# Kernel optimization log

Hardware: AMD Instinct MI355X
Metric: run time of the kernel (lower is better)

The kernel has to match this reference:

```python
import jax, jax.numpy as jnp
import numpy as np

WS = 7          # window size
SHIFT = 3       # shift size (SW-MSA)
NH = 4          # num heads
EPS = 1e-5      # LayerNorm eps (torch default)


def _rel_pos_index(ws):
    coords = np.stack(np.meshgrid(np.arange(ws), np.arange(ws), indexing='ij'))  # (2, ws, ws)
    cf = coords.reshape(2, -1)                      # (2, ws*ws)
    rel = cf[:, :, None] - cf[:, None, :]           # (2, N, N)
    rel = rel.transpose(1, 2, 0)
    rel[:, :, 0] += ws - 1
    rel[:, :, 1] += ws - 1
    rel[:, :, 0] *= 2 * ws - 1
    return jnp.asarray(rel.sum(-1))                 # (N, N) int

REL_IDX = _rel_pos_index(WS)


def _shift_mask(Hp, Wp, ws, shift):
    """Standard Swin attention mask for shifted windows: (nW, N, N) float32."""
    img = np.zeros((1, Hp, Wp, 1), dtype=np.float32)
    cnt = 0
    sl = (slice(0, -ws), slice(-ws, -shift), slice(-shift, None))
    for h in sl:
        for w in sl:
            img[:, h, w, :] = cnt
            cnt += 1
    win = img.reshape(1, Hp // ws, ws, Wp // ws, ws, 1).transpose(0, 1, 3, 2, 4, 5)
    win = win.reshape(-1, ws * ws)                  # (nW, N)
    m = win[:, None, :] - win[:, :, None]
    return jnp.asarray(np.where(m != 0, -100.0, 0.0).astype(np.float32))


def _ln(x, g, b):
    mu = jnp.mean(x, -1, keepdims=True)
    var = jnp.mean(jnp.square(x - mu), -1, keepdims=True)
    return (x - mu) * jax.lax.rsqrt(var + EPS) * g + b


def _win_partition(x, ws):
    B, H, W, C = x.shape
    x = x.reshape(B, H // ws, ws, W // ws, ws, C).transpose(0, 1, 3, 2, 4, 5)
    return x.reshape(-1, ws * ws, C)


def _win_reverse(w, ws, B, H, W):
    C = w.shape[-1]
    x = w.reshape(B, H // ws, W // ws, ws, ws, C).transpose(0, 1, 3, 2, 4, 5)
    return x.reshape(B, H, W, C)


def setup_inputs() -> dict:
    key = jax.random.key(0)
    ks = jax.random.split(key, 12)
    B, H, W, C = 16, 112, 112, 128
    hid = 4 * C
    std = 0.02
    inp = {
        'x': jax.random.normal(ks[0], (B, H * W, C), jnp.float32),
        'H': H, 'W': W,
        'attn_mask': _shift_mask(H, W, WS, SHIFT),
        'ln1_g': jnp.ones((C,), jnp.float32),
        'ln1_b': jnp.zeros((C,), jnp.float32),
        'qkv_w': jax.random.normal(ks[1], (3 * C, C), jnp.float32) * std,
        'qkv_b': jnp.zeros((3 * C,), jnp.float32),
        'rel_bias_table': jax.random.normal(ks[2], ((2 * WS - 1) ** 2, NH), jnp.float32) * std,
        'proj_w': jax.random.normal(ks[3], (C, C), jnp.float32) * std,
        'proj_b': jnp.zeros((C,), jnp.float32),
        'ln2_g': jnp.ones((C,), jnp.float32),
        'ln2_b': jnp.zeros((C,), jnp.float32),
        'fc1_w': jax.random.normal(ks[4], (hid, C), jnp.float32) * std,
        'fc1_b': jnp.zeros((hid,), jnp.float32),
        'fc2_w': jax.random.normal(ks[5], (C, hid), jnp.float32) * std,
        'fc2_b': jnp.zeros((C,), jnp.float32),
    }
    return inp


def reference(x, H, W, attn_mask, ln1_g, ln1_b, qkv_w, qkv_b, rel_bias_table,
              proj_w, proj_b, ln2_g, ln2_b, fc1_w, fc1_b, fc2_w, fc2_b):
    B, L, C = x.shape
    N = WS * WS
    hd = C // NH
    scale = hd ** -0.5

    shortcut = x
    h = _ln(x, ln1_g, ln1_b).reshape(B, H, W, C)
    # H, W chosen divisible by WS -> no padding branch needed
    h = jnp.roll(h, shift=(-SHIFT, -SHIFT), axis=(1, 2))
    xw = _win_partition(h, WS)                      # (B_, N, C), B_ = B*nW
    B_ = xw.shape[0]
    nW = attn_mask.shape[0]

    qkv = xw @ qkv_w.T + qkv_b                      # (B_, N, 3C)
    qkv = qkv.reshape(B_, N, 3, NH, hd).transpose(2, 0, 3, 1, 4)
    q, k, v = qkv[0], qkv[1], qkv[2]                # (B_, NH, N, hd)

    attn = jnp.einsum('bhnd,bhmd->bhnm', q, k) * scale
    bias = rel_bias_table[REL_IDX]                  # (N, N, NH)
    attn = attn + bias.transpose(2, 0, 1)[None]     # (B_, NH, N, N)
    attn = attn.reshape(B_ // nW, nW, NH, N, N) + attn_mask[None, :, None]
    attn = jax.nn.softmax(attn.reshape(B_, NH, N, N), axis=-1)

    o = jnp.einsum('bhnm,bhmd->bhnd', attn, v)      # (B_, NH, N, hd)
    o = o.transpose(0, 2, 1, 3).reshape(B_, N, C)
    o = o @ proj_w.T + proj_b

    h = _win_reverse(o, WS, B, H, W)
    h = jnp.roll(h, shift=(SHIFT, SHIFT), axis=(1, 2))
    x1 = shortcut + h.reshape(B, L, C)

    f = _ln(x1, ln2_g, ln2_b)
    f = jax.nn.gelu(f @ fc1_w.T + fc1_b, approximate=False)
    f = f @ fc2_w.T + fc2_b
    return x1 + f
```

## Files before the change

kernel.cpp:

```cpp
#include <hip/hip_runtime.h>
#include <hip/hip_bf16.h>
#include <math.h>

#define B_IMG 16
#define HH 112
#define WW_ 112
#define CC 128
#define LL (HH*WW_)
#define BWIN 4096
#define NTOK 49
#define NROWS (BWIN*NTOK)
#define HD 32
#define SCALE 0.1767766952966369f
#define SHIFT_ 3

typedef short bf16x8 __attribute__((ext_vector_type(8)));
typedef float f32x4 __attribute__((ext_vector_type(4)));
typedef unsigned short ushort_t;

__device__ __forceinline__ float wave_sum(float v) {
#pragma unroll
  for (int off = 32; off >= 1; off >>= 1) v += __shfl_xor(v, off, 64);
  return v;
}

__global__ __launch_bounds__(256) void castw_kernel(const float* __restrict__ w,
                                                    __hip_bfloat16* __restrict__ o, int n) {
  int i = blockIdx.x * 256 + threadIdx.x;
  if (i < n) o[i] = __float2bfloat16(w[i]);
}

__global__ __launch_bounds__(256) void prep_bias(const float* __restrict__ table,
                                                 float* __restrict__ biasPad) {
  int idx = blockIdx.x * 256 + threadIdx.x;
  int h = idx >> 12, q = (idx >> 6) & 63, k = idx & 63;
  float v = 0.f;
  if (q < NTOK && k < NTOK) {
    int yi = q / 7, xi = q % 7, yj = k / 7, xj = k % 7;
    v = table[((yi - yj + 6) * 13 + (xi - xj + 6)) * 4 + h];
  }
  biasPad[idx] = v;
}

__global__ __launch_bounds__(256) void prep_mask(const float* __restrict__ mask,
                                                 float* __restrict__ maskPad) {
  int idx = blockIdx.x * 256 + threadIdx.x;
  int pat = idx >> 12, q = (idx >> 6) & 63, k = idx & 63;
  float v = -1e30f;
  if (q < NTOK && k < NTOK) v = mask[pat * (NTOK * NTOK) + q * NTOK + k];
  maskPad[idx] = v;
}

template<bool GATHER>
__global__ __launch_bounds__(256) void ln_kernel(
    const float* __restrict__ X, const float* __restrict__ g,
    const float* __restrict__ b, __hip_bfloat16* __restrict__ Y)
{
  int wid  = threadIdx.x >> 6;
  int lane = threadIdx.x & 63;
  int r = blockIdx.x * 4 + wid;
  size_t src;
  if (GATHER) {
    int win = r / NTOK, n = r % NTOK;
    int bi = win >> 8, wi = win & 255;
    int wh = wi >> 4, wwi = wi & 15;
    int ii = n / 7, jj = n % 7;
    int hp = wh * 7 + ii, wp = wwi * 7 + jj;
    int sh = (hp + SHIFT_) % HH, sw = (wp + SHIFT_) % WW_;
    src = ((size_t)bi * LL + (size_t)sh * WW_ + sw) * CC;
  } else {
    src = (size_t)r * CC;
  }
  float v0 = X[src + lane];
  float v1 = X[src + 64 + lane];
  float mean = wave_sum(v0 + v1) * (1.f / CC);
  float d0 = v0 - mean, d1 = v1 - mean;
  float var = wave_sum(d0 * d0 + d1 * d1) * (1.f / CC);
  float rstd = rsqrtf(var + 1e-5f);
  size_t dst = (size_t)r * CC;
  Y[dst + lane]      = __float2bfloat16(d0 * rstd * g[lane]      + b[lane]);
  Y[dst + 64 + lane] = __float2bfloat16(d1 * rstd * g[lane + 64] + b[lane + 64]);
}

enum { EPI_BIAS = 0, EPI_GELU = 1, EPI_RES = 2, EPI_PROJ = 3 };
#define LDSW 136

template<int EPI>
__global__ __launch_bounds__(256, 2) void gemm_bf16(
    const ushort_t* __restrict__ A, const ushort_t* __restrict__ W,
    const float* __restrict__ bias, const float* __restrict__ aux,
    void* __restrict__ outp, int N, int K)
{
  __shared__ ushort_t As[128 * LDSW];
  __shared__ ushort_t Bs[128 * LDSW];
  int t = threadIdx.x;
  int lane = t & 63;
  int quad = lane >> 4;
  int l16  = lane & 15;
  int wr = (t >> 7) * 64;
  int wc = ((t >> 6) & 1) * 64;
  int m0 = blockIdx.x * 128, n0 = blockIdx.y * 128;

  f32x4 acc[4][4];
#pragma unroll
  for (int i = 0; i < 4; ++i)
#pragma unroll
    for (int j = 0; j < 4; ++j) acc[i][j] = (f32x4){0.f, 0.f, 0.f, 0.f};

  for (int kb = 0; kb < K; kb += 128) {
    if (kb) __syncthreads();
#pragma unroll
    for (int p = 0; p < 8; ++p) {
      int lin = p * 256 + t;
      int row = lin >> 4;
      int col = (lin & 15) * 8;
      uint4 av = *(const uint4*)(A + (size_t)(m0 + row) * K + kb + col);
      uint4 bv = *(const uint4*)(W + (size_t)(n0 + row) * K + kb + col);
      *(uint4*)&As[row * LDSW + col] = av;
      *(uint4*)&Bs[row * LDSW + col] = bv;
    }
    __syncthreads();
#pragma unroll
    for (int ks = 0; ks < 4; ++ks) {
      int k0 = ks * 32 + quad * 8;
      bf16x8 af[4], bf[4];
#pragma unroll
      for (int i = 0; i < 4; ++i)
        af[i] = *(const bf16x8*)&As[(wr + i * 16 + l16) * LDSW + k0];
#pragma unroll
      for (int j = 0; j < 4; ++j)
        bf[j] = *(const bf16x8*)&Bs[(wc + j * 16 + l16) * LDSW + k0];
#pragma unroll
      for (int i = 0; i < 4; ++i)
#pragma unroll
        for (int j = 0; j < 4; ++j)
          acc[i][j] = __builtin_amdgcn_mfma_f32_16x16x32_bf16(af[i], bf[j], acc[i][j], 0, 0, 0);
    }
  }

#pragma unroll
  for (int i = 0; i < 4; ++i) {
#pragma unroll
    for (int j = 0; j < 4; ++j) {
      int n = n0 + wc + j * 16 + l16;
      float bn = bias[n];
#pragma unroll
      for (int reg = 0; reg < 4; ++reg) {
        int m = m0 + wr + i * 16 + quad * 4 + reg;
        float v = acc[i][j][reg] + bn;
        if (EPI == EPI_BIAS) {
          ((__hip_bfloat16*)outp)[(size_t)m * N + n] = __float2bfloat16(v);
        } else if (EPI == EPI_GELU) {
          v = 0.5f * v * (1.f + erff(v * 0.70710678118654752f));
          ((__hip_bfloat16*)outp)[(size_t)m * N + n] = __float2bfloat16(v);
        } else if (EPI == EPI_RES) {
          ((float*)outp)[(size_t)m * N + n] = v + aux[(size_t)m * N + n];
        } else {
          int win = m / NTOK, nn = m % NTOK;
          int bi = win >> 8, wi = win & 255;
          int wh = wi >> 4, wwi = wi & 15;
          int ii = nn / 7, jj = nn % 7;
          int hp = wh * 7 + ii, wp = wwi * 7 + jj;
          int oh = (hp + SHIFT_) % HH, ow = (wp + SHIFT_) % WW_;
          size_t idx = ((size_t)bi * LL + (size_t)oh * WW_ + ow) * CC + n;
          ((float*)outp)[idx] = aux[idx] + v;
        }
      }
    }
  }
}

#define WLDS 6656

__global__ __launch_bounds__(256) void attn_mfma(
    const ushort_t* __restrict__ qkv, const float* __restrict__ maskPad,
    const float* __restrict__ biasPad, __hip_bfloat16* __restrict__ O, int win_off)
{
  __shared__ ushort_t lds[4 * WLDS];
  const int win_l = blockIdx.x;
  const int win_g = win_off + win_l;
  const int h    = threadIdx.x >> 6;
  const int lane = threadIdx.x & 63;
  const int quad = lane >> 4;
  const int l16  = lane & 15;
  ushort_t* wb = lds + h * WLDS;
  ushort_t* Vt = wb + 4608;

  {
    const int tok = lane;
    uint4 z = make_uint4(0u, 0u, 0u, 0u);
    uint4 k0 = z, k1 = z, k2 = z, k3 = z;
    union { uint4 v4[4]; ushort_t u[32]; } vv;
    vv.v4[0] = z; vv.v4[1] = z; vv.v4[2] = z; vv.v4[3] = z;
    if (tok < NTOK) {
      const ushort_t* src = qkv + ((size_t)win_l * NTOK + tok) * 384 + h * HD;
      k0 = *(const uint4*)(src + 128); k1 = *(const uint4*)(src + 136);
      k2 = *(const uint4*)(src + 144); k3 = *(const uint4*)(src + 152);
      vv.v4[0] = *(const uint4*)(src + 256); vv.v4[1] = *(const uint4*)(src + 264);
      vv.v4[2] = *(const uint4*)(src + 272); vv.v4[3] = *(const uint4*)(src + 280);
    }
    *(uint4*)&wb[tok * 40 +  0] = k0;
    *(uint4*)&wb[tok * 40 +  8] = k1;
    *(uint4*)&wb[tok * 40 + 16] = k2;
    *(uint4*)&wb[tok * 40 + 24] = k3;
#pragma unroll
    for (int d = 0; d < 32; ++d) Vt[d * 64 + tok] = vv.u[d];
  }

  bf16x8 qf[4];
  {
    const ushort_t* qb = qkv + (size_t)win_l * NTOK * 384 + h * HD + quad * 8;
#pragma unroll
    for (int i = 0; i < 4; ++i)
      qf[i] = *(const bf16x8*)(qb + (size_t)(i * 16 + l16) * 384);
  }

  f32x4 S[4][4];
#pragma unroll
  for (int i = 0; i < 4; ++i)
#pragma unroll
    for (int j = 0; j < 4; ++j) S[i][j] = (f32x4){0.f, 0.f, 0.f, 0.f};
  bf16x8 kf[4];
#pragma unroll
  for (int j = 0; j < 4; ++j)
    kf[j] = *(const bf16x8*)&wb[(j * 16 + l16) * 40 + quad * 8];
#pragma unroll
  for (int i = 0; i < 4; ++i)
#pragma unroll
    for (int j = 0; j < 4; ++j)
      S[i][j] = __builtin_amdgcn_mfma_f32_16x16x32_bf16(qf[i], kf[j], S[i][j], 0, 0, 0);

  const float* mrow = maskPad + (size_t)(win_g & 255) * 4096;
  const float* brow = biasPad + (size_t)h * 4096;
#pragma unroll
  for (int i = 0; i < 4; ++i)
#pragma unroll
    for (int j = 0; j < 4; ++j)
#pragma unroll
      for (int r = 0; r < 4; ++r) {
        int q = i * 16 + quad * 4 + r;
        int k = j * 16 + l16;
        S[i][j][r] = fmaf(S[i][j][r], SCALE, brow[q * 64 + k] + mrow[q * 64 + k]);
      }

  float inv[4][4];
#pragma unroll
  for (int i = 0; i < 4; ++i)
#pragma unroll
    for (int r = 0; r < 4; ++r) {
      float mx = fmaxf(fmaxf(S[i][0][r], S[i][1][r]), fmaxf(S[i][2][r], S[i][3][r]));
      mx = fmaxf(mx, __shfl_xor(mx, 1, 64));
      mx = fmaxf(mx, __shfl_xor(mx, 2, 64));
      mx = fmaxf(mx, __shfl_xor(mx, 4, 64));
      mx = fmaxf(mx, __shfl_xor(mx, 8, 64));
      float sum = 0.f;
#pragma unroll
      for (int j = 0; j < 4; ++j) {
        float e = __expf(S[i][j][r] - mx);
        S[i][j][r] = e;
        sum += e;
      }
      sum += __shfl_xor(sum, 1, 64);
      sum += __shfl_xor(sum, 2, 64);
      sum += __shfl_xor(sum, 4, 64);
      sum += __shfl_xor(sum, 8, 64);
      inv[i][r] = 1.f / sum;
    }

#pragma unroll
  for (int i = 0; i < 4; ++i)
#pragma unroll
    for (int j = 0; j < 4; ++j)
#pragma unroll
      for (int r = 0; r < 4; ++r) {
        int q = i * 16 + quad * 4 + r;
        int k = j * 16 + l16;
        *(__hip_bfloat16*)&wb[q * 72 + k] = __float2bfloat16(S[i][j][r]);
      }

  f32x4 Oacc[4][2];
#pragma unroll
  for (int i = 0; i < 4; ++i) {
    Oacc[i][0] = (f32x4){0.f, 0.f, 0.f, 0.f};
    Oacc[i][1] = (f32x4){0.f, 0.f, 0.f, 0.f};
  }
  bf16x8 vf[2][2];
#pragma unroll
  for (int ks = 0; ks < 2; ++ks)
#pragma unroll
    for (int jp = 0; jp < 2; ++jp)
      vf[ks][jp] = *(const bf16x8*)&Vt[(jp * 16 + l16) * 64 + ks * 32 + quad * 8];
#pragma unroll
  for (int i = 0; i < 4; ++i)
#pragma unroll
    for (int ks = 0; ks < 2; ++ks) {
      bf16x8 pf = *(const bf16x8*)&wb[(i * 16 + l16) * 72 + ks * 32 + quad * 8];
#pragma unroll
      for (int jp = 0; jp < 2; ++jp)
        Oacc[i][jp] = __builtin_amdgcn_mfma_f32_16x16x32_bf16(pf, vf[ks][jp], Oacc[i][jp], 0, 0, 0);
    }

  __hip_bfloat16* ob = O + ((size_t)win_g * NTOK) * CC + h * HD;
#pragma unroll
  for (int i = 0; i < 4; ++i)
#pragma unroll
    for (int r = 0; r < 4; ++r) {
      int q = i * 16 + quad * 4 + r;
      if (q < NTOK) {
        float s = inv[i][r];
#pragma unroll
        for (int jp = 0; jp < 2; ++jp)
          ob[(size_t)q * CC + jp * 16 + l16] = __float2bfloat16(Oacc[i][jp][r] * s);
      }
    }
}

extern "C" void kernel_launch(void* const* d_in, const int* in_sizes, int n_in,
                              void* d_out, int out_size, void* d_ws, size_t ws_size,
                              hipStream_t stream) {
  const float* x        = (const float*)d_in[0];
  const float* attnmask = (const float*)d_in[3];
  const float* ln1_g    = (const float*)d_in[4];
  const float* ln1_b    = (const float*)d_in[5];
  const float* qkv_w    = (const float*)d_in[6];
  const float* qkv_b    = (const float*)d_in[7];
  const float* table    = (const float*)d_in[8];
  const float* proj_w   = (const float*)d_in[9];
  const float* proj_b   = (const float*)d_in[10];
  const float* ln2_g    = (const float*)d_in[11];
  const float* ln2_b    = (const float*)d_in[12];
  const float* fc1_w    = (const float*)d_in[13];
  const float* fc1_b    = (const float*)d_in[14];
  const float* fc2_w    = (const float*)d_in[15];
  const float* fc2_b    = (const float*)d_in[16];
  float* out = (float*)d_out;

  __hip_bfloat16* bufA = (__hip_bfloat16*)d_ws;
  __hip_bfloat16* bufB = bufA + (size_t)NROWS * CC;
  __hip_bfloat16* wq   = bufB + (size_t)(NROWS / 2) * 384;
  __hip_bfloat16* wp   = wq + 384 * 128;
  __hip_bfloat16* w1   = wp + 128 * 128;
  __hip_bfloat16* w2   = w1 + 512 * 128;
  float* biasPad = (float*)(w2 + 128 * 512);
  float* maskPad = biasPad + 4 * 4096;

  castw_kernel<<<(384 * 128 + 255) / 256, 256, 0, stream>>>(qkv_w, wq, 384 * 128);
  castw_kernel<<<(128 * 128 + 255) / 256, 256, 0, stream>>>(proj_w, wp, 128 * 128);
  castw_kernel<<<(512 * 128 + 255) / 256, 256, 0, stream>>>(fc1_w, w1, 512 * 128);
  castw_kernel<<<(128 * 512 + 255) / 256, 256, 0, stream>>>(fc2_w, w2, 128 * 512);
  prep_bias<<<64, 256, 0, stream>>>(table, biasPad);
  prep_mask<<<4096, 256, 0, stream>>>(attnmask, maskPad);

  ln_kernel<true><<<NROWS / 4, 256, 0, stream>>>(x, ln1_g, ln1_b, bufA);

  for (int c = 0; c < 2; ++c) {
    const int MC = NROWS / 2;
    const ushort_t* Ain = (const ushort_t*)(bufA + (size_t)c * MC * CC);
    dim3 g(MC / 128, 384 / 128);
    gemm_bf16<EPI_BIAS><<<g, 256, 0, stream>>>(Ain, (const ushort_t*)wq, qkv_b,
                                               nullptr, bufB, 384, 128);
    attn_mfma<<<2048, 256, 0, stream>>>((const ushort_t*)bufB, maskPad, biasPad,
                                        bufA, c * 2048);
  }

  {
    dim3 g(NROWS / 128, 1);
    gemm_bf16<EPI_PROJ><<<g, 256, 0, stream>>>((const ushort_t*)bufA, (const ushort_t*)wp,
                                               proj_b, x, out, 128, 128);
  }
  ln_kernel<false><<<NROWS / 4, 256, 0, stream>>>(out, ln2_g, ln2_b, bufA);

  for (int c = 0; c < 4; ++c) {
    const int MC = NROWS / 4;
    const ushort_t* Ain = (const ushort_t*)(bufA + (size_t)c * MC * CC);
    float* Oc = out + (size_t)c * MC * CC;
    dim3 g1(MC / 128, 512 / 128);
    gemm_bf16<EPI_GELU><<<g1, 256, 0, stream>>>(Ain, (const ushort_t*)w1, fc1_b,
                                                nullptr, bufB, 512, 128);
    dim3 g2(MC / 128, 1);
    gemm_bf16<EPI_RES><<<g2, 256, 0, stream>>>((const ushort_t*)bufB, (const ushort_t*)w2,
                                               fc2_b, Oc, Oc, 128, 512);
  }
}
```

Measured before the change: 652.5 us.

## Fuse LN2 into proj GEMM, reuse A tile across N blocks, unchunk pipeline

The GEMM now loops over all N-blocks inside one workgroup for the QKV and FC1 GEMMs (K=128). The A tile stays resident in LDS while only the weight tile is restaged, which avoids rereading A once per N-block. When the workspace is large enough, the proj GEMM computes the second LayerNorm in its epilogue via shuffle and LDS reductions, which removes the separate LN kernel and its reread of the residual. The chunked launches are also collapsed into single full-size launches. The trade-off is fewer blocks, with serialized N work per block and a single-pass variance formula.

```diff
diff --git a/kernel.cpp b/kernel.cpp
--- a/kernel.cpp
+++ b/kernel.cpp
@@ -85,11 +85,52 @@
 enum { EPI_BIAS = 0, EPI_GELU = 1, EPI_RES = 2, EPI_PROJ = 3 };
 #define LDSW 136
 
-template<int EPI>
+#define STAGE_A(KB)                                                              \
+  _Pragma("unroll")                                                              \
+  for (int p = 0; p < 8; ++p) {                                                  \
+    int lin = p * 256 + t;                                                       \
+    int row = lin >> 4;                                                          \
+    int col = (lin & 15) * 8;                                                    \
+    *(uint4*)&As[row * LDSW + col] =                                             \
+        *(const uint4*)(A + (size_t)(m0 + row) * K + (KB) + col);                \
+  }
+
+#define STAGE_B(NOFF, KB)                                                        \
+  _Pragma("unroll")                                                              \
+  for (int p = 0; p < 8; ++p) {                                                  \
+    int lin = p * 256 + t;                                                       \
+    int row = lin >> 4;                                                          \
+    int col = (lin & 15) * 8;                                                    \
+    *(uint4*)&Bs[row * LDSW + col] =                                             \
+        *(const uint4*)(W + (size_t)((NOFF) + row) * K + (KB) + col);            \
+  }
+
+#define MFMA_BLOCK                                                               \
+  _Pragma("unroll")                                                              \
+  for (int ks = 0; ks < 4; ++ks) {                                               \
+    int k0 = ks * 32 + quad * 8;                                                 \
+    bf16x8 af[4], bf[4];                                                         \
+    _Pragma("unroll")                                                            \
+    for (int i = 0; i < 4; ++i)                                                  \
+      af[i] = *(const bf16x8*)&As[(wr + i * 16 + l16) * LDSW + k0];              \
+    _Pragma("unroll")                                                            \
+    for (int j = 0; j < 4; ++j)                                                  \
+      bf[j] = *(const bf16x8*)&Bs[(wc + j * 16 + l16) * LDSW + k0];              \
+    _Pragma("unroll")                                                            \
+    for (int i = 0; i < 4; ++i)                                                  \
+      _Pragma("unroll")                                                          \
+      for (int j = 0; j < 4; ++j)                                                \
+        acc[i][j] = __builtin_amdgcn_mfma_f32_16x16x32_bf16(af[i], bf[j],        \
+                                                            acc[i][j], 0, 0, 0); \
+  }
+
+template<int EPI, int NB, bool LNF>
 __global__ __launch_bounds__(256, 2) void gemm_bf16(
     const ushort_t* __restrict__ A, const ushort_t* __restrict__ W,
     const float* __restrict__ bias, const float* __restrict__ aux,
-    void* __restrict__ outp, int N, int K)
+    void* __restrict__ outp, const float* __restrict__ g2,
+    const float* __restrict__ b2, __hip_bfloat16* __restrict__ ln_out,
+    int N, int K)
 {
   __shared__ ushort_t As[128 * LDSW];
   __shared__ ushort_t Bs[128 * LDSW];
@@ -99,71 +140,132 @@
   int l16  = lane & 15;
   int wr = (t >> 7) * 64;
   int wc = ((t >> 6) & 1) * 64;
-  int m0 = blockIdx.x * 128, n0 = blockIdx.y * 128;
+  int m0 = blockIdx.x * 128;
 
   f32x4 acc[4][4];
-#pragma unroll
-  for (int i = 0; i < 4; ++i)
-#pragma unroll
-    for (int j = 0; j < 4; ++j) acc[i][j] = (f32x4){0.f, 0.f, 0.f, 0.f};
-
-  for (int kb = 0; kb < K; kb += 128) {
-    if (kb) __syncthreads();
-#pragma unroll
-    for (int p = 0; p < 8; ++p) {
-      int lin = p * 256 + t;
-      int row = lin >> 4;
-      int col = (lin & 15) * 8;
-      uint4 av = *(const uint4*)(A + (size_t)(m0 + row) * K + kb + col);
-      uint4 bv = *(const uint4*)(W + (size_t)(n0 + row) * K + kb + col);
-      *(uint4*)&As[row * LDSW + col] = av;
-      *(uint4*)&Bs[row * LDSW + col] = bv;
-    }
-    __syncthreads();
-#pragma unroll
-    for (int ks = 0; ks < 4; ++ks) {
-      int k0 = ks * 32 + quad * 8;
-      bf16x8 af[4], bf[4];
-#pragma unroll
-      for (int i = 0; i < 4; ++i)
-        af[i] = *(const bf16x8*)&As[(wr + i * 16 + l16) * LDSW + k0];
-#pragma unroll
-      for (int j = 0; j < 4; ++j)
-        bf[j] = *(const bf16x8*)&Bs[(wc + j * 16 + l16) * LDSW + k0];
-#pragma unroll
-      for (int i = 0; i < 4; ++i)
-#pragma unroll
-        for (int j = 0; j < 4; ++j)
-          acc[i][j] = __builtin_amdgcn_mfma_f32_16x16x32_bf16(af[i], bf[j], acc[i][j], 0, 0, 0);
-    }
-  }
-
-#pragma unroll
-  for (int i = 0; i < 4; ++i) {
-#pragma unroll
-    for (int j = 0; j < 4; ++j) {
-      int n = n0 + wc + j * 16 + l16;
-      float bn = bias[n];
-#pragma unroll
-      for (int reg = 0; reg < 4; ++reg) {
-        int m = m0 + wr + i * 16 + quad * 4 + reg;
-        float v = acc[i][j][reg] + bn;
-        if (EPI == EPI_BIAS) {
-          ((__hip_bfloat16*)outp)[(size_t)m * N + n] = __float2bfloat16(v);
-        } else if (EPI == EPI_GELU) {
-          v = 0.5f * v * (1.f + erff(v * 0.70710678118654752f));
-          ((__hip_bfloat16*)outp)[(size_t)m * N + n] = __float2bfloat16(v);
-        } else if (EPI == EPI_RES) {
-          ((float*)outp)[(size_t)m * N + n] = v + aux[(size_t)m * N + n];
-        } else {
+
+  for (int nb = 0; nb < NB; ++nb) {
+    int n_off = (NB == 1) ? blockIdx.y * 128 : nb * 128;
+#pragma unroll
+    for (int i = 0; i < 4; ++i)
+#pragma unroll
+      for (int j = 0; j < 4; ++j) acc[i][j] = (f32x4){0.f, 0.f, 0.f, 0.f};
+
+    if (NB == 1) {
+      for (int kb = 0; kb < K; kb += 128) {
+        if (kb) __syncthreads();
+        STAGE_A(kb);
+        STAGE_B(n_off, kb);
+        __syncthreads();
+        MFMA_BLOCK;
+      }
+    } else {
+      if (nb == 0) { STAGE_A(0); STAGE_B(0, 0); }
+      __syncthreads();
+      MFMA_BLOCK;
+      __syncthreads();
+      if (nb + 1 < NB) { STAGE_B((nb + 1) * 128, 0); }
+    }
+
+    if (EPI == EPI_PROJ) {
+      float s[4][4], ss[4][4];
+      unsigned rowB[4][4];
+#pragma unroll
+      for (int i = 0; i < 4; ++i) {
+#pragma unroll
+        for (int r = 0; r < 4; ++r) {
+          s[i][r] = 0.f; ss[i][r] = 0.f;
+          int m = m0 + wr + i * 16 + quad * 4 + r;
           int win = m / NTOK, nn = m % NTOK;
           int bi = win >> 8, wi = win & 255;
           int wh = wi >> 4, wwi = wi & 15;
           int ii = nn / 7, jj = nn % 7;
           int hp = wh * 7 + ii, wp = wwi * 7 + jj;
           int oh = (hp + SHIFT_) % HH, ow = (wp + SHIFT_) % WW_;
-          size_t idx = ((size_t)bi * LL + (size_t)oh * WW_ + ow) * CC + n;
-          ((float*)outp)[idx] = aux[idx] + v;
+          unsigned base = ((unsigned)bi * LL + (unsigned)oh * WW_ + ow) * CC;
+          rowB[i][r] = base;
+#pragma unroll
+          for (int j = 0; j < 4; ++j) {
+            int n = wc + j * 16 + l16;
+            float x1 = aux[base + n] + acc[i][j][r] + bias[n];
+            ((float*)outp)[base + n] = x1;
+            if (LNF) {
+              acc[i][j][r] = x1;
+              s[i][r] += x1;
+              ss[i][r] = fmaf(x1, x1, ss[i][r]);
+            }
+          }
+        }
+      }
+      if (LNF) {
+#pragma unroll
+        for (int i = 0; i < 4; ++i)
+#pragma unroll
+          for (int r = 0; r < 4; ++r) {
+#pragma unroll
+            for (int off = 8; off >= 1; off >>= 1) {
+              s[i][r]  += __shfl_xor(s[i][r],  off, 64);
+              ss[i][r] += __shfl_xor(ss[i][r], off, 64);
+            }
+          }
+        float* red = (float*)As;
+        __syncthreads();
+        if (l16 == 0) {
+#pragma unroll
+          for (int i = 0; i < 4; ++i)
+#pragma unroll
+            for (int r = 0; r < 4; ++r) {
+              int ml = wr + i * 16 + quad * 4 + r;
+              red[((wc >> 6) * 128 + ml) * 2 + 0] = s[i][r];
+              red[((wc >> 6) * 128 + ml) * 2 + 1] = ss[i][r];
+            }
+        }
+        __syncthreads();
+#pragma unroll
+        for (int i = 0; i < 4; ++i)
+#pragma unroll
+          for (int r = 0; r < 4; ++r) {
+            int ml = wr + i * 16 + quad * 4 + r;
+            float st  = red[ml * 2 + 0] + red[(128 + ml) * 2 + 0];
+            float sst = red[ml * 2 + 1] + red[(128 + ml) * 2 + 1];
+            float mean = st * (1.f / 128.f);
+            float var  = sst * (1.f / 128.f) - mean * mean;
+            s[i][r]  = mean;
+            ss[i][r] = rsqrtf(var + 1e-5f);
+          }
+#pragma unroll
+        for (int i = 0; i < 4; ++i)
+#pragma unroll
+          for (int r = 0; r < 4; ++r) {
+            unsigned base = rowB[i][r];
+#pragma unroll
+            for (int j = 0; j < 4; ++j) {
+              int n = wc + j * 16 + l16;
+              float ln = (acc[i][j][r] - s[i][r]) * ss[i][r] * g2[n] + b2[n];
+              ln_out[(size_t)base + n] = __float2bfloat16(ln);
+            }
+          }
+      }
+    } else {
+#pragma unroll
+      for (int i = 0; i < 4; ++i) {
+#pragma unroll
+        for (int j = 0; j < 4; ++j) {
+          int n = n_off + wc + j * 16 + l16;
+          float bn = bias[n];
+#pragma unroll
+          for (int reg = 0; reg < 4; ++reg) {
+            int m = m0 + wr + i * 16 + quad * 4 + reg;
+            float v = acc[i][j][reg] + bn;
+            if (EPI == EPI_BIAS) {
+              ((__hip_bfloat16*)outp)[(size_t)m * N + n] = __float2bfloat16(v);
+            } else if (EPI == EPI_GELU) {
+              v = 0.5f * v * (1.f + erff(v * 0.70710678118654752f));
+              ((__hip_bfloat16*)outp)[(size_t)m * N + n] = __float2bfloat16(v);
+            } else {
+              ((float*)outp)[(size_t)m * N + n] = v + aux[(size_t)m * N + n];
+            }
+          }
         }
       }
     }
@@ -307,10 +409,10 @@
     for (int r = 0; r < 4; ++r) {
       int q = i * 16 + quad * 4 + r;
       if (q < NTOK) {
-        float s = inv[i][r];
+        float sc = inv[i][r];
 #pragma unroll
         for (int jp = 0; jp < 2; ++jp)
-          ob[(size_t)q * CC + jp * 16 + l16] = __float2bfloat16(Oacc[i][jp][r] * s);
+          ob[(size_t)q * CC + jp * 16 + l16] = __float2bfloat16(Oacc[i][jp][r] * sc);
       }
     }
 }
@@ -335,9 +437,27 @@
   const float* fc2_b    = (const float*)d_in[16];
   float* out = (float*)d_out;
 
+  const size_t bufA_elems = (size_t)NROWS * CC;
+  const size_t bufB_full  = (size_t)NROWS * 512;
+  const size_t bufB_chunk = (size_t)(NROWS / 2) * 384;
+  const size_t bufC_elems = (size_t)NROWS * CC;
+  const size_t w_elems    = 384*128 + 128*128 + 512*128 + 128*512;
+  const size_t tbl_floats = 4 * 4096 + 256 * 4096;
+  const size_t need_full  =
+      (bufA_elems + bufB_full + bufC_elems + w_elems) * 2 + tbl_floats * 4;
+  const bool full = ws_size >= need_full;
+
   __hip_bfloat16* bufA = (__hip_bfloat16*)d_ws;
-  __hip_bfloat16* bufB = bufA + (size_t)NROWS * CC;
-  __hip_bfloat16* wq   = bufB + (size_t)(NROWS / 2) * 384;
+  __hip_bfloat16* bufB = bufA + bufA_elems;
+  __hip_bfloat16* bufC;
+  __hip_bfloat16* wq;
+  if (full) {
+    bufC = bufB + bufB_full;
+    wq   = bufC + bufC_elems;
+  } else {
+    bufC = nullptr;
+    wq   = bufB + bufB_chunk;
+  }
   __hip_bfloat16* wp   = wq + 384 * 128;
   __hip_bfloat16* w1   = wp + 128 * 128;
   __hip_bfloat16* w2   = w1 + 512 * 128;
@@ -353,32 +473,52 @@
 
   ln_kernel<true><<<NROWS / 4, 256, 0, stream>>>(x, ln1_g, ln1_b, bufA);
 
-  for (int c = 0; c < 2; ++c) {
-    const int MC = NROWS / 2;
-    const ushort_t* Ain = (const ushort_t*)(bufA + (size_t)c * MC * CC);
-    dim3 g(MC / 128, 384 / 128);
-    gemm_bf16<EPI_BIAS><<<g, 256, 0, stream>>>(Ain, (const ushort_t*)wq, qkv_b,
-                                               nullptr, bufB, 384, 128);
-    attn_mfma<<<2048, 256, 0, stream>>>((const ushort_t*)bufB, maskPad, biasPad,
-                                        bufA, c * 2048);
-  }
-
-  {
+  if (full) {
     dim3 g(NROWS / 128, 1);
-    gemm_bf16<EPI_PROJ><<<g, 256, 0, stream>>>((const ushort_t*)bufA, (const ushort_t*)wp,
-                                               proj_b, x, out, 128, 128);
-  }
-  ln_kernel<false><<<NROWS / 4, 256, 0, stream>>>(out, ln2_g, ln2_b, bufA);
-
-  for (int c = 0; c < 4; ++c) {
-    const int MC = NROWS / 4;
-    const ushort_t* Ain = (const ushort_t*)(bufA + (size_t)c * MC * CC);
-    float* Oc = out + (size_t)c * MC * CC;
-    dim3 g1(MC / 128, 512 / 128);
-    gemm_bf16<EPI_GELU><<<g1, 256, 0, stream>>>(Ain, (const ushort_t*)w1, fc1_b,
-                                                nullptr, bufB, 512, 128);
-    dim3 g2(MC / 128, 1);
-    gemm_bf16<EPI_RES><<<g2, 256, 0, stream>>>((const ushort_t*)bufB, (const ushort_t*)w2,
-                                               fc2_b, Oc, Oc, 128, 512);
-  }
-}
+    gemm_bf16<EPI_BIAS, 3, false><<<g, 256, 0, stream>>>(
+        (const ushort_t*)bufA, (const ushort_t*)wq, qkv_b, nullptr, bufB,
+        nullptr, nullptr, nullptr, 384, 128);
+    attn_mfma<<<BWIN, 256, 0, stream>>>((const ushort_t*)bufB, maskPad, biasPad,
+                                        bufA, 0);
+    gemm_bf16<EPI_PROJ, 1, true><<<g, 256, 0, stream>>>(
+        (const ushort_t*)bufA, (const ushort_t*)wp, proj_b, x, out,
+        ln2_g, ln2_b, bufC, 128, 128);
+    gemm_bf16<EPI_GELU, 4, false><<<g, 256, 0, stream>>>(
+        (const ushort_t*)bufC, (const ushort_t*)w1, fc1_b, nullptr, bufB,
+        nullptr, nullptr, nullptr, 512, 128);
+    gemm_bf16<EPI_RES, 1, false><<<g, 256, 0, stream>>>(
+        (const ushort_t*)bufB, (const ushort_t*)w2, fc2_b, out, out,
+        nullptr, nullptr, nullptr, 128, 512);
+  } else {
+    for (int c = 0; c < 2; ++c) {
+      const int MC = NROWS / 2;
+      const ushort_t* Ain = (const ushort_t*)(bufA + (size_t)c * MC * CC);
+      dim3 g(MC / 128, 1);
+      gemm_bf16<EPI_BIAS, 3, false><<<g, 256, 0, stream>>>(
+          Ain, (const ushort_t*)wq, qkv_b, nullptr, bufB,
+          nullptr, nullptr, nullptr, 384, 128);
+      attn_mfma<<<2048, 256, 0, stream>>>((const ushort_t*)bufB, maskPad, biasPad,
+                                          bufA, c * 2048);
+    }
+    {
+      dim3 g(NROWS / 128, 1);
+      gemm_bf16<EPI_PROJ, 1, false><<<g, 256, 0, stream>>>(
+          (const ushort_t*)bufA, (const ushort_t*)wp, proj_b, x, out,
+          nullptr, nullptr, nullptr, 128, 128);
+    }
+    ln_kernel<false><<<NROWS / 4, 256, 0, stream>>>(out, ln2_g, ln2_b, bufA);
+    for (int c = 0; c < 4; ++c) {
+      const int MC = NROWS / 4;
+      const ushort_t* Ain = (const ushort_t*)(bufA + (size_t)c * MC * CC);
+      float* Oc = out + (size_t)c * MC * CC;
+      dim3 g1(MC / 128, 1);
+      gemm_bf16<EPI_GELU, 4, false><<<g1, 256, 0, stream>>>(
+          Ain, (const ushort_t*)w1, fc1_b, nullptr, bufB,
+          nullptr, nullptr, nullptr, 512, 128);
+      dim3 g2(MC / 128, 1);
+      gemm_bf16<EPI_RES, 1, false><<<g2, 256, 0, stream>>>(
+          (const ushort_t*)bufB, (const ushort_t*)w2, fc2_b, Oc, Oc,
+          nullptr, nullptr, nullptr, 128, 512);
+    }
+  }
+}
```

New measurement: 612.6 us. 6.1% less time.
